# Kernel tuning notes

Hardware: AMD Instinct MI355X
Metric: run time of the kernel (lower is better)

The kernel has to match this reference:

```python
import jax, jax.numpy as jnp
import numpy as np

NUM_CATEGORIES = 16
INPUT_DIM = 1024
HIDDEN_DIM = 4096
BATCH = 64
SEQ = 256


def setup_inputs() -> dict:
    key = jax.random.key(0)
    k1, k2, k3 = jax.random.split(key, 3)
    x = jax.random.normal(k1, (BATCH, SEQ, INPUT_DIM), dtype=jnp.float32)
    cat_ids = jax.random.randint(k2, (BATCH,), 0, NUM_CATEGORIES, dtype=jnp.int64)
    W = 0.02 * jax.random.normal(k3, (NUM_CATEGORIES, INPUT_DIM, HIDDEN_DIM), dtype=jnp.float32)
    b = jnp.zeros((NUM_CATEGORIES, HIDDEN_DIM), dtype=jnp.float32)
    return {"x": x, "cat_ids": cat_ids, "W": W, "b": b}


def reference(x, cat_ids, W, b):
    # Gather per-sample expert weights then batched matmul, matching torch.bmm semantics.
    selected_W = W[cat_ids]            # [B, input_dim, hidden_dim]
    selected_b = b[cat_ids]            # [B, hidden_dim]
    out = jnp.einsum('bsi,bih->bsh', x, selected_W) + selected_b[:, None, :]
    return out
```

## Files before the change

kernel.cpp:

```cpp
#include <hip/hip_runtime.h>
#include <hip/hip_bf16.h>
#include <stdint.h>

#define BATCH 64
#define SEQ   256
#define KDIM  1024
#define NDIM  4096
#define NCAT  16

#define BM 256
#define BN 256
#define BK 64
#define NT_G (NDIM/BN)
#define KT_G (KDIM/BK)
#define GEMM_BLOCKS (BATCH*NT_G)

typedef __attribute__((ext_vector_type(4))) float f32x4;
typedef __attribute__((ext_vector_type(4))) unsigned int u32x4;
typedef __attribute__((ext_vector_type(8))) short bf16x8;

__device__ __forceinline__ unsigned short f2bf(float f) {
  __hip_bfloat16 h = __float2bfloat16(f);
  return __builtin_bit_cast(unsigned short, h);
}
__device__ __forceinline__ unsigned pack2(float lo, float hi) {
  return (unsigned)f2bf(lo) | ((unsigned)f2bf(hi) << 16);
}
__device__ __forceinline__ void gload16(const void* g, void* l) {
  __builtin_amdgcn_global_load_lds(
      (const __attribute__((address_space(1))) unsigned int*)g,
      (__attribute__((address_space(3))) unsigned int*)l, 16, 0, 0);
}


#define CVT_W_BLOCKS (NCAT*(KDIM/64)*(NDIM/64))
#define CVT_X_BLOCKS ((BATCH*SEQ*KDIM/8)/256)

__global__ void cvt_fused(const float* __restrict__ x,
                          const float* __restrict__ W,
                          unsigned char* __restrict__ xb_t,
                          unsigned char* __restrict__ Wt) {
  __shared__ float ls[64][65];
  const int tid = threadIdx.x;

  if (blockIdx.x < CVT_W_BLOCKS) {
    const int bid = blockIdx.x;
    const int cat = bid >> 10;
    const int rem = bid & 1023;
    const int kt  = rem >> 6;
    const int ntl = rem & 63;

    const float* src = W + (size_t)cat * KDIM * NDIM + (size_t)(kt * 64) * NDIM + ntl * 64;
    const int kl = tid >> 4;
    const int nl = (tid & 15) * 4;
#pragma unroll
    for (int i = 0; i < 4; ++i) {
      f32x4 v = *(const f32x4*)(src + (size_t)(kl + i * 16) * NDIM + nl);
      ls[kl + i * 16][nl + 0] = v[0];
      ls[kl + i * 16][nl + 1] = v[1];
      ls[kl + i * 16][nl + 2] = v[2];
      ls[kl + i * 16][nl + 3] = v[3];
    }
    __syncthreads();
    const int n  = tid >> 2;
    const int k2 = (tid & 3) * 16;
    u32x4 q0, q1;
#pragma unroll
    for (int j = 0; j < 4; ++j) q0[j] = pack2(ls[k2 + 2 * j][n],     ls[k2 + 2 * j + 1][n]);
#pragma unroll
    for (int j = 0; j < 4; ++j) q1[j] = pack2(ls[k2 + 8 + 2 * j][n], ls[k2 + 9 + 2 * j][n]);

    const int nt   = ntl >> 2;
    const int sub  = ntl & 3;
    const int h    = sub >> 1;
    const int r    = (sub & 1) * 64 + n;
    const unsigned sw = ((unsigned)r & 7u) << 4;
    unsigned base = (unsigned)(cat * 8388608) + (unsigned)(nt * 524288)
                  + (unsigned)((kt * 2 + h) * 16384) + (unsigned)(r * 128);
    *(u32x4*)(Wt + base + (((unsigned)(k2 * 2))      ^ sw)) = q0;
    *(u32x4*)(Wt + base + (((unsigned)(k2 * 2 + 16)) ^ sw)) = q1;
  } else {
    int g = (blockIdx.x - CVT_W_BLOCKS) * 256 + tid;
    const int row = g >> 7;
    const int c   = g & 127;
    const int b   = row >> 8;
    const int s   = row & 255;
    const int kt  = c >> 3;
    const int ck  = c & 7;
    const int h   = s >> 7;
    const int r   = s & 127;
    const float* src = x + (size_t)row * KDIM + c * 8;
    f32x4 a = *(const f32x4*)src;
    f32x4 d = *(const f32x4*)(src + 4);
    u32x4 q;
    q[0] = pack2(a[0], a[1]); q[1] = pack2(a[2], a[3]);
    q[2] = pack2(d[0], d[1]); q[3] = pack2(d[2], d[3]);
    unsigned off = (unsigned)(((b * 16 + kt) * 2 + h) * 16384)
                 + (unsigned)(r * 128) + (((unsigned)(ck * 16)) ^ (((unsigned)r & 7u) << 4));
    *(u32x4*)(xb_t + off) = q;
  }
}

__global__ __launch_bounds__(512, 2)
void csl_gemm(const unsigned char* __restrict__ xb_t,
              const unsigned char* __restrict__ Wt,
              const int*   __restrict__ cat_ids,
              const float* __restrict__ bias,
              float* __restrict__ out)
{
  __shared__ __align__(16) unsigned char lds[131072];
  __shared__ int s_cat[BATCH];

  const int tid  = threadIdx.x;
  const int lane = tid & 63;
  const int wid  = tid >> 6;
  const int wm   = wid >> 2;
  const int wn   = wid & 3;

  if (tid < BATCH) s_cat[tid] = cat_ids[tid];
  __syncthreads();

  const int bid  = (int)blockIdx.x;
  const int t_id = (bid & 7) * (GEMM_BLOCKS / 8) + (bid >> 3);

  const int myc = s_cat[lane];
  int c = 0, base = 0, cc = 0;
  unsigned long long mask = 0ULL;
  for (c = 0; c < NCAT; ++c) {
    mask = __ballot(myc == c);
    cc = __popcll(mask);
    int sz = cc * NT_G;
    if (t_id < base + sz) break;
    base += sz;
  }
  if (c >= NCAT) return;
  const int idx = t_id - base;
  const int nt  = idx / cc;
  const int pos = idx % cc;
  unsigned long long mm = mask;
  for (int i = 0; i < pos; ++i) mm &= (mm - 1);
  const int batch = __ffsll((long long)mm) - 1;
  const int cat   = c;

  const unsigned char* Ab = xb_t + (size_t)batch * 524288;
  const unsigned char* Bb = Wt  + (size_t)cat * 8388608 + (size_t)nt * 524288;

  const unsigned tb16 = (unsigned)(tid * 16);

#define STAGE_A(kt, h)                                                     \
  {                                                                        \
    const unsigned char* g = Ab + (unsigned)(((kt) * 2 + (h)) * 16384) + tb16; \
    unsigned char* l = lds + (((kt) & 1) * 65536) + ((h) * 16384) + tb16;  \
    gload16(g, l); gload16(g + 8192, l + 8192);                            \
  }
#define STAGE_B(kt, h)                                                     \
  {                                                                        \
    const unsigned char* g = Bb + (unsigned)(((kt) * 2 + (h)) * 16384) + tb16; \
    unsigned char* l = lds + (((kt) & 1) * 65536) + 32768 + ((h) * 16384) + tb16; \
    gload16(g, l); gload16(g + 8192, l + 8192);                            \
  }

  const int lc       = lane & 15;
  const unsigned sw  = ((unsigned)lc & 7u) << 4;
  const unsigned kq16 = (unsigned)((lane >> 4) * 16);
  const unsigned koff0 = kq16 ^ sw;
  const unsigned koff1 = (64u + kq16) ^ sw;
  const unsigned bA = (unsigned)(wm * 16384 + lc * 128);
  const unsigned bB = 32768u + (unsigned)((wn >> 1) * 16384 + (wn & 1) * 8192 + lc * 128);
#define KOFF(kk) ((kk) ? koff1 : koff0)

  f32x4 acc[8][4] = {};
  bf16x8 bfr[4];

#define PHASE(mh, kk, DOB, EXTRA)                                          \
  {                                                                        \
    if (DOB) {                                                             \
      _Pragma("unroll")                                                    \
      for (int ni = 0; ni < 4; ++ni)                                       \
        bfr[ni] = *(const bf16x8*)(lds + pb + bB + (unsigned)(ni * 2048) + KOFF(kk)); \
    }                                                                      \
    bf16x8 af[4];                                                          \
    _Pragma("unroll")                                                      \
    for (int mi = 0; mi < 4; ++mi)                                         \
      af[mi] = *(const bf16x8*)(lds + pb + bA + (unsigned)((mh) * 8192 + mi * 2048) + KOFF(kk)); \
    EXTRA                                                                  \
    __builtin_amdgcn_s_barrier();                                          \
    asm volatile("s_waitcnt lgkmcnt(0)" ::: "memory");                     \
    __builtin_amdgcn_sched_barrier(0);                                     \
    __builtin_amdgcn_s_setprio(1);                                         \
    _Pragma("unroll")                                                      \
    for (int mi = 0; mi < 4; ++mi)                                         \
      _Pragma("unroll")                                                    \
      for (int ni = 0; ni < 4; ++ni)                                       \
        acc[(mh) * 4 + mi][ni] = __builtin_amdgcn_mfma_f32_16x16x32_bf16(  \
            af[mi], bfr[ni], acc[(mh) * 4 + mi][ni], 0, 0, 0);             \
    __builtin_amdgcn_s_setprio(0);                                         \
    __builtin_amdgcn_s_barrier();                                          \
  }

#define PHASE_TAIL(mh, kk, STAGECODE, VMCODE)                              \
  {                                                                        \
    bf16x8 af[4];                                                          \
    _Pragma("unroll")                                                      \
    for (int mi = 0; mi < 4; ++mi)                                         \
      af[mi] = *(const bf16x8*)(lds + pb + bA + (unsigned)((mh) * 8192 + mi * 2048) + KOFF(kk)); \
    asm volatile("s_waitcnt lgkmcnt(0)" ::: "memory");                     \
    __builtin_amdgcn_sched_barrier(0);                                     \
    __builtin_amdgcn_s_barrier();                                          \
    STAGECODE                                                              \
    VMCODE                                                                 \
    __builtin_amdgcn_sched_barrier(0);                                     \
    __builtin_amdgcn_s_setprio(1);                                         \
    _Pragma("unroll")                                                      \
    for (int mi = 0; mi < 4; ++mi)                                         \
      _Pragma("unroll")                                                    \
      for (int ni = 0; ni < 4; ++ni)                                       \
        acc[(mh) * 4 + mi][ni] = __builtin_amdgcn_mfma_f32_16x16x32_bf16(  \
            af[mi], bfr[ni], acc[(mh) * 4 + mi][ni], 0, 0, 0);             \
    __builtin_amdgcn_s_setprio(0);                                         \
    __builtin_amdgcn_s_barrier();                                          \
  }

  STAGE_A(0, 0); STAGE_A(0, 1); STAGE_B(0, 0); STAGE_B(0, 1);
  STAGE_A(1, 0); STAGE_A(1, 1); STAGE_B(1, 0);
  asm volatile("s_waitcnt vmcnt(6)" ::: "memory");
  __builtin_amdgcn_s_barrier();

  for (int t = 0; t < KT_G; ++t) {
    const unsigned pb = (unsigned)((t & 1) * 65536);
    PHASE(0, 0, 1, { if (t + 1 < KT_G) STAGE_B(t + 1, 1); })
    PHASE(1, 0, 0, {})
    PHASE(0, 1, 1, {})
    if (t + 2 < KT_G) {
      PHASE_TAIL(1, 1,
        { STAGE_A(t + 2, 0); STAGE_A(t + 2, 1); STAGE_B(t + 2, 0); },
        { asm volatile("s_waitcnt vmcnt(6)" ::: "memory"); })
    } else if (t + 2 == KT_G) {
      PHASE_TAIL(1, 1, {}, { asm volatile("s_waitcnt vmcnt(0)" ::: "memory"); })
    } else {
      PHASE_TAIL(1, 1, {}, {})
    }
  }

  const int col_l = lane & 15;
  const int row_l = (lane >> 4) * 4;
#pragma unroll
  for (int mf = 0; mf < 8; ++mf) {
#pragma unroll
    for (int ni = 0; ni < 4; ++ni) {
      int gr = wm * 128 + mf * 16 + row_l;
      int gc = nt * BN + wn * 64 + ni * 16 + col_l;
      float bvl = bias[(size_t)cat * NDIM + gc];
      f32x4 v = acc[mf][ni];
      size_t o = ((size_t)batch * SEQ + gr) * NDIM + gc;
      out[o]            = v[0] + bvl;
      out[o + NDIM]     = v[1] + bvl;
      out[o + 2 * NDIM] = v[2] + bvl;
      out[o + 3 * NDIM] = v[3] + bvl;
    }
  }
#undef PHASE
#undef PHASE_TAIL
#undef KOFF
#undef STAGE_A
#undef STAGE_B
}

#define FBM 128
#define FBN 128
#define FBK 64
#define FMT (SEQ/FBM)
#define FNT (NDIM/FBN)
#define FTPB (FMT*FNT)
#define FNB (BATCH*FTPB)
typedef __attribute__((ext_vector_type(2))) unsigned int u32x2;

__global__ __launch_bounds__(256, 2)
void csl_fallback(const float* __restrict__ x,
                  const int*   __restrict__ cat_ids,
                  const float* __restrict__ W,
                  const float* __restrict__ bias,
                  float* __restrict__ out)
{
  __shared__ __align__(16) unsigned char sA[FBM * FBK * 2];
  __shared__ __align__(16) unsigned char sB[FBN * FBK * 2];
  __shared__ int s_cat[BATCH];

  const int tid  = threadIdx.x;
  const int lane = tid & 63;
  const int wid  = tid >> 6;

  if (tid < BATCH) s_cat[tid] = cat_ids[tid];
  __syncthreads();

  const int myc = s_cat[lane];
  int t_id = (int)blockIdx.x;
  int c = 0, base = 0, cc = 0;
  unsigned long long mask = 0ULL;
  for (c = 0; c < NCAT; ++c) {
    mask = __ballot(myc == c);
    cc = __popcll(mask);
    int sz = cc * FTPB;
    if (t_id < base + sz) break;
    base += sz;
  }
  if (c >= NCAT) return;
  const int idx    = t_id - base;
  const int per_nt = cc * FMT;
  const int nt     = idx / per_nt;
  const int r      = idx % per_nt;
  const int want   = r >> 1;
  const int mt     = r & 1;
  unsigned long long mm = mask;
  for (int i = 0; i < want; ++i) mm &= (mm - 1);
  const int batch = __ffsll((long long)mm) - 1;
  const int cat   = c;

  const int m0 = mt * FBM;
  const int n0 = nt * FBN;

  const size_t x_base = ((size_t)batch * SEQ + m0) * KDIM;
  const size_t w_base = (size_t)cat * KDIM * NDIM + n0;

  f32x4 acc[4][4] = {};
  const int wr = (wid >> 1) * 64;
  const int wc = (wid & 1) * 64;

  for (int kt = 0; kt < KDIM / FBK; ++kt) {
    const int k0 = kt * FBK;
    f32x4 av[4][2];
#pragma unroll
    for (int s = 0; s < 4; ++s) {
      int seg  = tid + s * 256;
      int arow = seg >> 3;
      int ak   = (seg & 7) << 3;
      const float* gp = x + x_base + (size_t)arow * KDIM + (size_t)(k0 + ak);
      av[s][0] = *(const f32x4*)gp;
      av[s][1] = *(const f32x4*)(gp + 4);
    }
    f32x4 bv[2][4];
#pragma unroll
    for (int s = 0; s < 2; ++s) {
      int u  = tid + s * 256;
      int nq = u & 31;
      int kq = u >> 5;
      const float* gp = W + w_base + (size_t)(k0 + kq * 4) * NDIM + (size_t)(nq * 4);
#pragma unroll
      for (int rr = 0; rr < 4; ++rr)
        bv[s][rr] = *(const f32x4*)(gp + (size_t)rr * NDIM);
    }
    __syncthreads();
#pragma unroll
    for (int s = 0; s < 4; ++s) {
      int seg  = tid + s * 256;
      int arow = seg >> 3;
      int akb  = (seg & 7) << 4;
      unsigned byte = (unsigned)(arow * (FBK * 2)) + ((unsigned)akb ^ (((unsigned)arow & 7u) << 4));
      u32x4 q;
      q[0] = pack2(av[s][0][0], av[s][0][1]);
      q[1] = pack2(av[s][0][2], av[s][0][3]);
      q[2] = pack2(av[s][1][0], av[s][1][1]);
      q[3] = pack2(av[s][1][2], av[s][1][3]);
      *(u32x4*)(sA + byte) = q;
    }
#pragma unroll
    for (int s = 0; s < 2; ++s) {
      int u  = tid + s * 256;
      int nq = u & 31;
      int kq = u >> 5;
      unsigned swz = ((unsigned)nq & 7u) << 4;
#pragma unroll
      for (int i = 0; i < 4; ++i) {
        int n = nq * 4 + i;
        unsigned byte = (unsigned)(n * (FBK * 2)) + (((unsigned)(kq * 8)) ^ swz);
        u32x2 d;
        d[0] = pack2(bv[s][0][i], bv[s][1][i]);
        d[1] = pack2(bv[s][2][i], bv[s][3][i]);
        *(u32x2*)(sB + byte) = d;
      }
    }
    __syncthreads();
#pragma unroll
    for (int kk = 0; kk < 2; ++kk) {
      const int kb = kk * 64 + ((lane >> 4) << 4);
      bf16x8 af[4], bfr[4];
#pragma unroll
      for (int mi = 0; mi < 4; ++mi) {
        int row = wr + mi * 16 + (lane & 15);
        unsigned byte = (unsigned)(row * (FBK * 2)) + ((unsigned)kb ^ (((unsigned)row & 7u) << 4));
        af[mi] = *(const bf16x8*)(sA + byte);
      }
#pragma unroll
      for (int ni = 0; ni < 4; ++ni) {
        int n = wc + ni * 16 + (lane & 15);
        unsigned byte = (unsigned)(n * (FBK * 2)) + ((unsigned)kb ^ ((((unsigned)n >> 2) & 7u) << 4));
        bfr[ni] = *(const bf16x8*)(sB + byte);
      }
#pragma unroll
      for (int mi = 0; mi < 4; ++mi)
#pragma unroll
        for (int ni = 0; ni < 4; ++ni)
          acc[mi][ni] = __builtin_amdgcn_mfma_f32_16x16x32_bf16(af[mi], bfr[ni], acc[mi][ni], 0, 0, 0);
    }
  }

  const int col_l = lane & 15;
  const int row_l = (lane >> 4) * 4;
#pragma unroll
  for (int mi = 0; mi < 4; ++mi) {
#pragma unroll
    for (int ni = 0; ni < 4; ++ni) {
      int gr = m0 + wr + mi * 16 + row_l;
      int gc = n0 + wc + ni * 16 + col_l;
      float bvl = bias[(size_t)cat * NDIM + gc];
      f32x4 v = acc[mi][ni];
      size_t o = ((size_t)batch * SEQ + gr) * NDIM + gc;
      out[o]            = v[0] + bvl;
      out[o + NDIM]     = v[1] + bvl;
      out[o + 2 * NDIM] = v[2] + bvl;
      out[o + 3 * NDIM] = v[3] + bvl;
    }
  }
}

extern "C" void kernel_launch(void* const* d_in, const int* in_sizes, int n_in,
                              void* d_out, int out_size, void* d_ws, size_t ws_size,
                              hipStream_t stream) {
  const float* x       = (const float*)d_in[0];
  const int*   cat_ids = (const int*)d_in[1];
  const float* W       = (const float*)d_in[2];
  const float* bias    = (const float*)d_in[3];
  float*       out     = (float*)d_out;
  (void)in_sizes; (void)n_in; (void)out_size;

  const size_t wt_bytes = (size_t)NCAT * NDIM * KDIM * 2;
  const size_t xb_bytes = (size_t)BATCH * SEQ * KDIM * 2;
  const size_t need = wt_bytes + xb_bytes;

  if (ws_size >= need) {
    unsigned char* Wt   = (unsigned char*)d_ws;
    unsigned char* xb_t = Wt + wt_bytes;
    hipLaunchKernelGGL(cvt_fused, dim3(CVT_W_BLOCKS + CVT_X_BLOCKS), dim3(256), 0, stream,
                       x, W, xb_t, Wt);
    hipLaunchKernelGGL(csl_gemm, dim3(GEMM_BLOCKS), dim3(512), 0, stream,
                       xb_t, Wt, cat_ids, bias, out);
  } else {
    hipLaunchKernelGGL(csl_fallback, dim3(FNB), dim3(256), 0, stream,
                       x, cat_ids, W, bias, out);
  }
}
```

Measured before the change: 304.5 us.

## Make GEMM blocks persistent over four tiles with cross-tile prefetch

Each workgroup now handles four consecutive output tiles rather than one, so the grid shrinks by four. During the last two k-steps of one tile it prefetches the first k-stages of the next tile into LDS, which hides pipeline fill and drain between tiles. Bias loads are hoisted per tile and accumulators are cleared after the epilogue. The tradeoffs are fewer blocks to balance across CUs (256 blocks at 2 per CU), and the epilogue stores now run serially inside the loop with the next tile's loads in flight.

```diff
diff --git a/kernel.cpp b/kernel.cpp
--- a/kernel.cpp
+++ b/kernel.cpp
@@ -13,7 +13,9 @@
 #define BK 64
 #define NT_G (NDIM/BN)
 #define KT_G (KDIM/BK)
-#define GEMM_BLOCKS (BATCH*NT_G)
+#define GEMM_TILES (BATCH*NT_G)
+#define TPB 4
+#define GEMM_BLOCKS (GEMM_TILES/TPB)
 
 typedef __attribute__((ext_vector_type(4))) float f32x4;
 typedef __attribute__((ext_vector_type(4))) unsigned int u32x4;
@@ -101,6 +103,29 @@
   }
 }
 
+struct TD { int batch, cat, nt; };
+
+__device__ __forceinline__ TD decode_tile(int t_id, int myc) {
+  TD td;
+  int c, base = 0, cc = 1;
+  unsigned long long mask = 0ULL;
+  for (c = 0; c < NCAT; ++c) {
+    mask = __ballot(myc == c);
+    cc = __popcll(mask);
+    int sz = cc * NT_G;
+    if (t_id < base + sz) break;
+    base += sz;
+  }
+  int idx = t_id - base;
+  td.cat = c;
+  td.nt  = idx / cc;
+  int pos = idx % cc;
+  unsigned long long mm = mask;
+  for (int i = 0; i < pos; ++i) mm &= (mm - 1);
+  td.batch = __ffsll((long long)mm) - 1;
+  return td;
+}
+
 __global__ __launch_bounds__(512, 2)
 void csl_gemm(const unsigned char* __restrict__ xb_t,
               const unsigned char* __restrict__ Wt,
@@ -119,49 +144,36 @@
 
   if (tid < BATCH) s_cat[tid] = cat_ids[tid];
   __syncthreads();
-
-  const int bid  = (int)blockIdx.x;
-  const int t_id = (bid & 7) * (GEMM_BLOCKS / 8) + (bid >> 3);
-
   const int myc = s_cat[lane];
-  int c = 0, base = 0, cc = 0;
-  unsigned long long mask = 0ULL;
-  for (c = 0; c < NCAT; ++c) {
-    mask = __ballot(myc == c);
-    cc = __popcll(mask);
-    int sz = cc * NT_G;
-    if (t_id < base + sz) break;
-    base += sz;
-  }
-  if (c >= NCAT) return;
-  const int idx = t_id - base;
-  const int nt  = idx / cc;
-  const int pos = idx % cc;
-  unsigned long long mm = mask;
-  for (int i = 0; i < pos; ++i) mm &= (mm - 1);
-  const int batch = __ffsll((long long)mm) - 1;
-  const int cat   = c;
-
-  const unsigned char* Ab = xb_t + (size_t)batch * 524288;
-  const unsigned char* Bb = Wt  + (size_t)cat * 8388608 + (size_t)nt * 524288;
+
+  const int bid = (int)blockIdx.x;
+  const int q   = (bid & 7) * (GEMM_BLOCKS / 8) + (bid >> 3);
+  const int t0  = q * TPB;
+
+  TD cur = decode_tile(t0, myc);
+  TD nxt = decode_tile(t0 + 1, myc);
+  const unsigned char* Ab  = xb_t + (size_t)cur.batch * 524288;
+  const unsigned char* Bb  = Wt  + (size_t)cur.cat * 8388608 + (size_t)cur.nt * 524288;
+  const unsigned char* AbN = xb_t + (size_t)nxt.batch * 524288;
+  const unsigned char* BbN = Wt  + (size_t)nxt.cat * 8388608 + (size_t)nxt.nt * 524288;
 
   const unsigned tb16 = (unsigned)(tid * 16);
 
-#define STAGE_A(kt, h)                                                     \
+#define STAGE_A(BASE, s, h)                                                \
   {                                                                        \
-    const unsigned char* g = Ab + (unsigned)(((kt) * 2 + (h)) * 16384) + tb16; \
-    unsigned char* l = lds + (((kt) & 1) * 65536) + ((h) * 16384) + tb16;  \
+    const unsigned char* g = (BASE) + (unsigned)(((s) * 2 + (h)) * 16384) + tb16; \
+    unsigned char* l = lds + (((s) & 1) * 65536) + ((h) * 16384) + tb16;   \
     gload16(g, l); gload16(g + 8192, l + 8192);                            \
   }
-#define STAGE_B(kt, h)                                                     \
+#define STAGE_B(BASE, s, h)                                                \
   {                                                                        \
-    const unsigned char* g = Bb + (unsigned)(((kt) * 2 + (h)) * 16384) + tb16; \
-    unsigned char* l = lds + (((kt) & 1) * 65536) + 32768 + ((h) * 16384) + tb16; \
+    const unsigned char* g = (BASE) + (unsigned)(((s) * 2 + (h)) * 16384) + tb16; \
+    unsigned char* l = lds + (((s) & 1) * 65536) + 32768 + ((h) * 16384) + tb16; \
     gload16(g, l); gload16(g + 8192, l + 8192);                            \
   }
 
-  const int lc       = lane & 15;
-  const unsigned sw  = ((unsigned)lc & 7u) << 4;
+  const int lc        = lane & 15;
+  const unsigned sw   = ((unsigned)lc & 7u) << 4;
   const unsigned kq16 = (unsigned)((lane >> 4) * 16);
   const unsigned koff0 = kq16 ^ sw;
   const unsigned koff1 = (64u + kq16) ^ sw;
@@ -221,42 +233,80 @@
     __builtin_amdgcn_s_barrier();                                          \
   }
 
-  STAGE_A(0, 0); STAGE_A(0, 1); STAGE_B(0, 0); STAGE_B(0, 1);
-  STAGE_A(1, 0); STAGE_A(1, 1); STAGE_B(1, 0);
+  STAGE_A(Ab, 0, 0); STAGE_A(Ab, 0, 1); STAGE_B(Bb, 0, 0); STAGE_B(Bb, 0, 1);
+  STAGE_A(Ab, 1, 0); STAGE_A(Ab, 1, 1); STAGE_B(Bb, 1, 0);
   asm volatile("s_waitcnt vmcnt(6)" ::: "memory");
   __builtin_amdgcn_s_barrier();
 
-  for (int t = 0; t < KT_G; ++t) {
-    const unsigned pb = (unsigned)((t & 1) * 65536);
-    PHASE(0, 0, 1, { if (t + 1 < KT_G) STAGE_B(t + 1, 1); })
-    PHASE(1, 0, 0, {})
-    PHASE(0, 1, 1, {})
-    if (t + 2 < KT_G) {
-      PHASE_TAIL(1, 1,
-        { STAGE_A(t + 2, 0); STAGE_A(t + 2, 1); STAGE_B(t + 2, 0); },
-        { asm volatile("s_waitcnt vmcnt(6)" ::: "memory"); })
-    } else if (t + 2 == KT_G) {
-      PHASE_TAIL(1, 1, {}, { asm volatile("s_waitcnt vmcnt(0)" ::: "memory"); })
-    } else {
-      PHASE_TAIL(1, 1, {}, {})
-    }
-  }
-
   const int col_l = lane & 15;
   const int row_l = (lane >> 4) * 4;
-#pragma unroll
-  for (int mf = 0; mf < 8; ++mf) {
-#pragma unroll
-    for (int ni = 0; ni < 4; ++ni) {
-      int gr = wm * 128 + mf * 16 + row_l;
-      int gc = nt * BN + wn * 64 + ni * 16 + col_l;
-      float bvl = bias[(size_t)cat * NDIM + gc];
-      f32x4 v = acc[mf][ni];
-      size_t o = ((size_t)batch * SEQ + gr) * NDIM + gc;
-      out[o]            = v[0] + bvl;
-      out[o + NDIM]     = v[1] + bvl;
-      out[o + 2 * NDIM] = v[2] + bvl;
-      out[o + 3 * NDIM] = v[3] + bvl;
+
+  for (int j = 0; j < TPB; ++j) {
+    const bool hn = (j + 1 < TPB);
+    for (int t = 0; t < KT_G - 2; ++t) {
+      const unsigned pb = (unsigned)((t & 1) * 65536);
+      PHASE(0, 0, 1, { STAGE_B(Bb, t + 1, 1); })
+      PHASE(1, 0, 0, {})
+      PHASE(0, 1, 1, {})
+      PHASE_TAIL(1, 1,
+        { STAGE_A(Ab, t + 2, 0); STAGE_A(Ab, t + 2, 1); STAGE_B(Bb, t + 2, 0); },
+        { asm volatile("s_waitcnt vmcnt(6)" ::: "memory"); })
+    }
+    {
+      const unsigned pb = 0;
+      PHASE(0, 0, 1, { STAGE_B(Bb, 15, 1); })
+      PHASE(1, 0, 0, {})
+      PHASE(0, 1, 1, {})
+      if (hn) {
+        PHASE_TAIL(1, 1,
+          { STAGE_A(AbN, 0, 0); STAGE_A(AbN, 0, 1); STAGE_B(BbN, 0, 0); },
+          { asm volatile("s_waitcnt vmcnt(6)" ::: "memory"); })
+      } else {
+        PHASE_TAIL(1, 1, {}, { asm volatile("s_waitcnt vmcnt(0)" ::: "memory"); })
+      }
+    }
+    {
+      const unsigned pb = 65536u;
+      if (hn) { PHASE(0, 0, 1, { STAGE_B(BbN, 0, 1); }) }
+      else    { PHASE(0, 0, 1, {}) }
+      PHASE(1, 0, 0, {})
+      PHASE(0, 1, 1, {})
+      if (hn) {
+        PHASE_TAIL(1, 1,
+          { STAGE_A(AbN, 1, 0); STAGE_A(AbN, 1, 1); STAGE_B(BbN, 1, 0); },
+          { asm volatile("s_waitcnt vmcnt(6)" ::: "memory"); })
+      } else {
+        PHASE_TAIL(1, 1, {}, {})
+      }
+    }
+    {
+      float bv4[4];
+#pragma unroll
+      for (int ni = 0; ni < 4; ++ni)
+        bv4[ni] = bias[(size_t)cur.cat * NDIM + cur.nt * BN + wn * 64 + ni * 16 + col_l];
+#pragma unroll
+      for (int mf = 0; mf < 8; ++mf) {
+#pragma unroll
+        for (int ni = 0; ni < 4; ++ni) {
+          int gr = wm * 128 + mf * 16 + row_l;
+          int gc = cur.nt * BN + wn * 64 + ni * 16 + col_l;
+          f32x4 v = acc[mf][ni];
+          size_t o = ((size_t)cur.batch * SEQ + gr) * NDIM + gc;
+          out[o]            = v[0] + bv4[ni];
+          out[o + NDIM]     = v[1] + bv4[ni];
+          out[o + 2 * NDIM] = v[2] + bv4[ni];
+          out[o + 3 * NDIM] = v[3] + bv4[ni];
+          acc[mf][ni] = (f32x4){0.f, 0.f, 0.f, 0.f};
+        }
+      }
+    }
+    if (hn) {
+      cur = nxt; Ab = AbN; Bb = BbN;
+      if (j + 2 < TPB) {
+        nxt = decode_tile(t0 + j + 2, myc);
+        AbN = xb_t + (size_t)nxt.batch * 524288;
+        BbN = Wt  + (size_t)nxt.cat * 8388608 + (size_t)nxt.nt * 524288;
+      }
     }
   }
 #undef PHASE
```

Measured after the change: 332.9 us. 9.3% more time.
